# Optimization experiments

Measured on AMD Instinct MI355X. Metric: run time of the kernel, lower is better.

## Reference

```python
import jax, jax.numpy as jnp
import numpy as np

N_QUBITS = 4
KERNEL = 4
STRIDE = 2
CDT = jnp.complex64


def _apply_mat(state, mat, wire):
    # state: (B,2,2,2,2); mat: (2,2) constant or (B,2,2) per-batch
    s = jnp.moveaxis(state, 1 + wire, -1)
    if mat.ndim == 3:
        s = jnp.einsum('bij,bklmj->bklmi', mat, s)
    else:
        s = jnp.einsum('ij,bklmj->bklmi', mat, s)
    return jnp.moveaxis(s, -1, 1 + wire)


def _apply_rz(state, theta, wire):
    # diagonal gate: multiply phases exp(-+ i theta/2) on target wire
    ph = jnp.exp(1j * (theta[:, None] * jnp.array([-0.5, 0.5], jnp.float32)))  # (B,2)
    s = jnp.moveaxis(state, 1 + wire, -1)
    s = s * ph[:, None, None, None, :]
    return jnp.moveaxis(s, -1, 1 + wire)


def _ry_mat(theta):
    c = jnp.cos(theta * 0.5)
    s = jnp.sin(theta * 0.5)
    return jnp.stack([jnp.stack([c, -s], -1), jnp.stack([s, c], -1)], -2).astype(CDT)


def _apply_crz(state, theta, ctrl, tgt):
    # controlled-RZ: phase only when control bit is 1
    e = jnp.exp(1j * (theta * jnp.array([-0.5, 0.5], jnp.float32)))  # (2,)
    ph = jnp.stack([jnp.ones(2, CDT), e.astype(CDT)])  # (2,2) indexed [ctrl_bit, tgt_bit]
    s = jnp.moveaxis(state, (1 + ctrl, 1 + tgt), (-2, -1))
    return jnp.moveaxis(s * ph, (-2, -1), (1 + ctrl, 1 + tgt))


def simulate(inputs, weights):
    # inputs: (B, L) angles per patch; weights: (n_layers, 2*n_qubits)
    B, L = inputs.shape
    vpq = L // N_QUBITS + 1  # var_per_qubit
    state = jnp.zeros((B, 2 ** N_QUBITS), CDT).at[:, 0].set(1.0).reshape(B, 2, 2, 2, 2)
    H = jnp.asarray([[1.0, 1.0], [1.0, -1.0]], CDT) * (1.0 / np.sqrt(2.0))
    # encoding: Hadamard then alternating RZ/RY per qubit
    for qub in range(N_QUBITS):
        state = _apply_mat(state, H, qub)
        for i in range(vpq):
            idx = qub * vpq + i
            if idx < L:
                theta = inputs[:, idx]
                if i % 2 == 0:
                    state = _apply_rz(state, theta, qub)
                else:
                    state = _apply_mat(state, _ry_mat(theta), qub)
    # variational layers
    n_layers = weights.shape[0]
    for l in range(n_layers):
        for i in range(N_QUBITS):
            state = _apply_crz(state, weights[l, i], i, (i + 1) % N_QUBITS)
        for j in range(N_QUBITS, 2 * N_QUBITS):
            state = _apply_mat(state, _ry_mat(weights[l, j]), j % N_QUBITS)
    # expval PauliZ on each wire
    probs = state.real ** 2 + state.imag ** 2  # (B,2,2,2,2)
    z = []
    for q in range(N_QUBITS):
        pq = jnp.moveaxis(probs, 1 + q, 1).reshape(B, 2, -1).sum(-1)  # (B,2)
        z.append(pq[:, 0] - pq[:, 1])
    return jnp.stack(z, -1)  # (B, n_qubits)


def setup_inputs() -> dict:
    key = jax.random.key(0)
    k1, k2 = jax.random.split(key)
    X = jax.random.uniform(k1, (64, 1, 128, 128), dtype=jnp.float32)
    weights = jax.random.uniform(k2, (1, 2 * N_QUBITS), dtype=jnp.float32)
    return {"X": X, "weights": weights}


def reference(X, weights):
    bs, C, Hh, Ww = X.shape
    ppd = (Hh - KERNEL) // STRIDE + 1
    rows = jnp.arange(ppd) * STRIDE
    win = jnp.arange(KERNEL)
    idx = rows[:, None] + win[None, :]  # (ppd, KERNEL)
    # extract all sliding patches at once: (bs, C, ppd, K, ppd, K)
    p = X[:, :, idx, :]          # (bs, C, ppd, K, W)
    p = p[..., idx]              # (bs, C, ppd, K, ppd, K)
    p = jnp.transpose(p, (0, 2, 4, 1, 3, 5))  # (bs, ppd_i, ppd_j, C, K, K)
    inputs = p.reshape(bs * ppd * ppd, C * KERNEL * KERNEL)
    z = simulate(inputs, weights)  # (bs*ppd*ppd, n_qubits)
    # replicate torch.cat(dim=1).view(bs, n_qubits, ppd, ppd)
    out = z.reshape(bs, ppd * ppd * N_QUBITS).reshape(bs, N_QUBITS, ppd, ppd)
    return out
```

## Files before the change

kernel.cpp:

```cpp
#include <hip/hip_runtime.h>
#include <math.h>

#define PPD 63
#define TOTAL (64*PPD*PPD)

__global__ void __launch_bounds__(256)
quanv_kernel(const float* __restrict__ X, const float* __restrict__ W,
             float* __restrict__ out) {
    __shared__ float2 crz[16];
    __shared__ float2 ryw[4];

    const int lt = threadIdx.x;
    if (lt < 16) {
        float phi = 0.f;
        #pragma unroll
        for (int i = 0; i < 4; ++i) {
            const int bi = (lt >> (3 - i)) & 1;
            const int bt = (lt >> (3 - ((i + 1) & 3))) & 1;
            if (bi) phi += (bt ? 0.5f : -0.5f) * W[i];
        }
        float s, c; __sincosf(phi, &s, &c);
        crz[lt] = make_float2(c, s);
    } else if (lt < 20) {
        const int q = lt - 16;
        float s, c; __sincosf(W[4 + q], &s, &c);
        ryw[q] = make_float2(0.0625f * c, 0.125f * s);
    }
    __syncthreads();

    const int tid = blockIdx.x * 256 + lt;
    if (tid >= TOTAL) return;

    const int b  = tid / (PPD * PPD);
    const int rc = tid - b * (PPD * PPD);
    const int r  = rc / PPD;
    const int c  = rc - r * PPD;

    const float2* xp = reinterpret_cast<const float2*>(
        X + b * (128 * 128) + (r * 2) * 128 + (c * 2));
    float th[16];
    #pragma unroll
    for (int i = 0; i < 4; ++i) {
        const float2 lo = xp[i * 64];
        const float2 hi = xp[i * 64 + 1];
        th[i*4+0] = lo.x; th[i*4+1] = lo.y;
        th[i*4+2] = hi.x; th[i*4+3] = hi.y;
    }

    float vx[3][2], vy[3][2];
    #pragma unroll
    for (int q = 0; q < 3; ++q) {
        float s0,c0,s1,c1,s2,c2,s3,c3,s4,c4;
        __sincosf(       th[q*5+0], &s0, &c0);
        __sincosf(0.5f * th[q*5+1], &s1, &c1);
        __sincosf(       th[q*5+2], &s2, &c2);
        __sincosf(0.5f * th[q*5+3], &s3, &c3);
        __sincosf(       th[q*5+4], &s4, &c4);
        const float v0x = c1 - s1*c0, v0y = -s1*s0;
        const float v1x = s1 + c1*c0, v1y =  c1*s0;
        const float w1x = v1x*c2 - v1y*s2, w1y = v1x*s2 + v1y*c2;
        const float n0x = c3*v0x - s3*w1x, n0y = c3*v0y - s3*w1y;
        const float n1x = s3*v0x + c3*w1x, n1y = s3*v0y + c3*w1y;
        vx[q][0] = n0x;               vy[q][0] = n0y;
        vx[q][1] = n1x*c4 - n1y*s4;   vy[q][1] = n1x*s4 + n1y*c4;
    }
    float ds_, dc_;
    __sincosf(th[15], &ds_, &dc_);

    float px[4], py[4];
    #pragma unroll
    for (int i = 0; i < 2; ++i)
        #pragma unroll
        for (int j = 0; j < 2; ++j) {
            px[i*2+j] = vx[0][i]*vx[1][j] - vy[0][i]*vy[1][j];
            py[i*2+j] = vx[0][i]*vy[1][j] + vy[0][i]*vx[1][j];
        }
    float qx[4], qy[4];
    #pragma unroll
    for (int i = 0; i < 2; ++i) {
        qx[i*2+0] = vx[2][i];
        qy[i*2+0] = vy[2][i];
        qx[i*2+1] = vx[2][i]*dc_ - vy[2][i]*ds_;
        qy[i*2+1] = vx[2][i]*ds_ + vy[2][i]*dc_;
    }

    float ax[16], ay[16];
    #pragma unroll
    for (int k = 0; k < 16; ++k) {
        const float tx = px[k>>2]*qx[k&3] - py[k>>2]*qy[k&3];
        const float ty = px[k>>2]*qy[k&3] + py[k>>2]*qx[k&3];
        const float2 t = crz[k];
        ax[k] = tx*t.x - ty*t.y;
        ay[k] = tx*t.y + ty*t.x;
    }

    float p[16];
    #pragma unroll
    for (int k = 0; k < 16; ++k) p[k] = ax[k]*ax[k] + ay[k]*ay[k];

    float z[4];
    #pragma unroll
    for (int q = 0; q < 4; ++q) {
        const int mask = 8 >> q;
        float zs = 0.f, xs = 0.f;
        #pragma unroll
        for (int k = 0; k < 16; ++k) {
            if (k & mask) continue;
            const int k1 = k | mask;
            zs += p[k] - p[k1];
            xs += ax[k]*ax[k1] + ay[k]*ay[k1];
        }
        const float2 w = ryw[q];
        z[q] = w.x * zs - w.y * xs;
    }

    reinterpret_cast<float4*>(out)[tid] = make_float4(z[0], z[1], z[2], z[3]);
}

extern "C" void kernel_launch(void* const* d_in, const int* in_sizes, int n_in,
                              void* d_out, int out_size, void* d_ws, size_t ws_size,
                              hipStream_t stream) {
    const float* X = (const float*)d_in[0];
    const float* W = (const float*)d_in[1];
    float* out = (float*)d_out;

    const int blocks = (TOTAL + 255) / 256;
    quanv_kernel<<<dim3(blocks), dim3(256), 0, stream>>>(X, W, out);
}
```

Measured before the change: 10.75 us.

## Compute qubit expectations in closed form from per-qubit product-state terms

Replaces the full 16-amplitude state construction, CRZ phase application and marginal sums with an algebraic closed form. It uses the product-state structure: each expectation depends only on per-qubit populations, coherences and neighbouring CRZ phases. This cuts arithmetic and register pressure per thread, and the block preamble shrinks to three small per-qubit tables. The risk is a mistake in the derived algebra, which would only be caught by the correctness check.

```diff
diff --git a/kernel.cpp b/kernel.cpp
--- a/kernel.cpp
+++ b/kernel.cpp
@@ -7,24 +7,19 @@
 __global__ void __launch_bounds__(256)
 quanv_kernel(const float* __restrict__ X, const float* __restrict__ W,
              float* __restrict__ out) {
-    __shared__ float2 crz[16];
-    __shared__ float2 ryw[4];
+    __shared__ float uA[4][2];
+    __shared__ float uB[4][2];
+    __shared__ float uR[4][2];
 
     const int lt = threadIdx.x;
-    if (lt < 16) {
-        float phi = 0.f;
-        #pragma unroll
-        for (int i = 0; i < 4; ++i) {
-            const int bi = (lt >> (3 - i)) & 1;
-            const int bt = (lt >> (3 - ((i + 1) & 3))) & 1;
-            if (bi) phi += (bt ? 0.5f : -0.5f) * W[i];
-        }
-        float s, c; __sincosf(phi, &s, &c);
-        crz[lt] = make_float2(c, s);
-    } else if (lt < 20) {
-        const int q = lt - 16;
-        float s, c; __sincosf(W[4 + q], &s, &c);
-        ryw[q] = make_float2(0.0625f * c, 0.125f * s);
+    if (lt < 4) {
+        float s, c;
+        __sincosf(0.5f * W[lt], &s, &c);
+        uA[lt][0] = c;        uA[lt][1] = 0.5f * s;
+        __sincosf(W[lt], &s, &c);
+        uB[lt][0] = c;        uB[lt][1] = s;
+        __sincosf(W[4 + lt], &s, &c);
+        uR[lt][0] = 0.5f * c; uR[lt][1] = 0.5f * s;
     }
     __syncthreads();
 
@@ -47,7 +42,7 @@
         th[i*4+2] = hi.x; th[i*4+3] = hi.y;
     }
 
-    float vx[3][2], vy[3][2];
+    float p0[4], p1[4], dr[4], mr[4], mi[4];
     #pragma unroll
     for (int q = 0; q < 3; ++q) {
         float s0,c0,s1,c1,s2,c2,s3,c3,s4,c4;
@@ -61,57 +56,31 @@
         const float w1x = v1x*c2 - v1y*s2, w1y = v1x*s2 + v1y*c2;
         const float n0x = c3*v0x - s3*w1x, n0y = c3*v0y - s3*w1y;
         const float n1x = s3*v0x + c3*w1x, n1y = s3*v0y + c3*w1y;
-        vx[q][0] = n0x;               vy[q][0] = n0y;
-        vx[q][1] = n1x*c4 - n1y*s4;   vy[q][1] = n1x*s4 + n1y*c4;
+        const float f1x = n1x*c4 - n1y*s4, f1y = n1x*s4 + n1y*c4;
+        const float P0 = n0x*n0x + n0y*n0y;
+        const float P1 = f1x*f1x + f1y*f1y;
+        p0[q] = P0; p1[q] = P1; dr[q] = P0 - P1;
+        mr[q] = n0x*f1x + n0y*f1y;
+        mi[q] = n0x*f1y - n0y*f1x;
     }
-    float ds_, dc_;
-    __sincosf(th[15], &ds_, &dc_);
-
-    float px[4], py[4];
-    #pragma unroll
-    for (int i = 0; i < 2; ++i)
-        #pragma unroll
-        for (int j = 0; j < 2; ++j) {
-            px[i*2+j] = vx[0][i]*vx[1][j] - vy[0][i]*vy[1][j];
-            py[i*2+j] = vx[0][i]*vy[1][j] + vy[0][i]*vx[1][j];
-        }
-    float qx[4], qy[4];
-    #pragma unroll
-    for (int i = 0; i < 2; ++i) {
-        qx[i*2+0] = vx[2][i];
-        qy[i*2+0] = vy[2][i];
-        qx[i*2+1] = vx[2][i]*dc_ - vy[2][i]*ds_;
-        qy[i*2+1] = vx[2][i]*ds_ + vy[2][i]*dc_;
+    {
+        float s, c; __sincosf(th[15], &s, &c);
+        p0[3] = 1.f; p1[3] = 1.f; dr[3] = 0.f;
+        mr[3] = c;   mi[3] = s;
     }
-
-    float ax[16], ay[16];
-    #pragma unroll
-    for (int k = 0; k < 16; ++k) {
-        const float tx = px[k>>2]*qx[k&3] - py[k>>2]*qy[k&3];
-        const float ty = px[k>>2]*qy[k&3] + py[k>>2]*qx[k&3];
-        const float2 t = crz[k];
-        ax[k] = tx*t.x - ty*t.y;
-        ay[k] = tx*t.y + ty*t.x;
-    }
-
-    float p[16];
-    #pragma unroll
-    for (int k = 0; k < 16; ++k) p[k] = ax[k]*ax[k] + ay[k]*ay[k];
 
     float z[4];
     #pragma unroll
     for (int q = 0; q < 4; ++q) {
-        const int mask = 8 >> q;
-        float zs = 0.f, xs = 0.f;
-        #pragma unroll
-        for (int k = 0; k < 16; ++k) {
-            if (k & mask) continue;
-            const int k1 = k | mask;
-            zs += p[k] - p[k1];
-            xs += ax[k]*ax[k1] + ay[k]*ay[k1];
-        }
-        const float2 w = ryw[q];
-        z[q] = w.x * zs - w.y * xs;
+        const int qn = (q + 1) & 3;
+        const int j  = (q + 3) & 3;
+        const float as_ = dr[qn] * uA[q][1];
+        const float br  = p0[j] + p1[j] * uB[j][0];
+        const float bi  = p1[j] * uB[j][1];
+        const float chw = uA[q][0];
+        const float re  = mr[q]*chw + mi[q]*as_;
+        const float im  = mi[q]*chw - mr[q]*as_;
+        z[q] = uR[q][0]*dr[q] - uR[q][1]*(re*br - im*bi);
     }
 
     reinterpret_cast<float4*>(out)[tid] = make_float4(z[0], z[1], z[2], z[3]);
```

Result: faster. 10.06 us (median of 2 runs) (-6.5%).
